# Kernel optimization log

Hardware: AMD Instinct MI355X
Metric: run time of the kernel (lower is better)

The kernel has to match this reference:

```python
import jax, jax.numpy as jnp
import numpy as np

N = 100000   # num nodes
E = 1200000  # num edges (avg degree ~12)
D = 64       # emb_dim


def setup_inputs() -> dict:
    key = jax.random.key(0)
    k1, k2, k3, k4, k5, k6 = jax.random.split(key, 6)
    x = jax.random.normal(k1, (N, D), dtype=jnp.float32)
    edge_index = jax.random.randint(k2, (2, E), 0, N, dtype=jnp.int64)
    edge_attr = jax.random.normal(k3, (E, D), dtype=jnp.float32)
    W = jax.random.normal(k4, (D, D), dtype=jnp.float32) * 0.05  # Linear weight
    b = jax.random.normal(k5, (D,), dtype=jnp.float32) * 0.05    # Linear bias
    root_emb = jax.random.normal(k6, (D,), dtype=jnp.float32)
    return {"x": x, "edge_index": edge_index, "edge_attr": edge_attr,
            "W": W, "b": b, "root_emb": root_emb}


def reference(x, edge_index, edge_attr, W, b, root_emb):
    n = x.shape[0]
    x = x @ W.T + b  # Linear(emb_dim, emb_dim)
    row, col = edge_index[0], edge_index[1]
    ones_e = jnp.ones(row.shape[0], dtype=x.dtype)
    # degrees initialized to ones then index_add of ones per edge endpoint
    deg_i = 1.0 + jax.ops.segment_sum(ones_e, row, num_segments=n)
    deg_j = 1.0 + jax.ops.segment_sum(ones_e, col, num_segments=n)
    dinv_i = deg_i ** -0.5
    dinv_j = deg_j ** -0.5
    val = dinv_i[row] * dinv_j[col]  # [E] normalized edge weights
    # spmm(adj_t, x) + message_edge both scatter val-weighted terms to `row`;
    # fuse into a single gather->scale->segment_sum pass (identical math).
    agg = jax.ops.segment_sum(val[:, None] * (x[col] + edge_attr), row,
                              num_segments=n)  # [N, D]
    node_feat = jax.nn.relu(agg) + jax.nn.relu(x + root_emb) * (dinv_i * dinv_j)[:, None]
    return node_feat
```

## Files before the change

### kernel.cpp

```cpp
#include <hip/hip_runtime.h>

#define N_NODES 100000
#define N_EDGES 1200000
#define DIM     64
#define SCAN_B  256
#define NB      ((N_NODES + SCAN_B - 1) / SCAN_B)
#define LIN_ROWS   32
#define LIN_BLOCKS (N_NODES / LIN_ROWS)
#define CNT_BLOCKS ((N_EDGES / 4 + 255) / 256)

typedef unsigned short ushort_t;
typedef float f4 __attribute__((ext_vector_type(4)));

__device__ inline float bf2f(ushort_t u) {
    return __uint_as_float(((unsigned int)u) << 16);
}
__device__ inline ushort_t f2bf(float f) {
    unsigned int x = __float_as_uint(f);
    unsigned int r = x + 0x7fff + ((x >> 16) & 1);
    return (ushort_t)(r >> 16);
}

__global__ __launch_bounds__(256) void prep_kernel(
        const float* __restrict__ x, const float* __restrict__ W,
        const float* __restrict__ b, ushort_t* __restrict__ xwb,
        const int* __restrict__ row, const int* __restrict__ col,
        int* __restrict__ cnt_r, int* __restrict__ cnt_c,
        int* __restrict__ rank) {
    __shared__ float sWt[DIM * (DIM + 1)];
    __shared__ f4    sx4[LIN_ROWS][DIM / 4];

    int t = threadIdx.x;

    if (blockIdx.x >= LIN_BLOCKS) {
        int i = (blockIdx.x - LIN_BLOCKS) * 256 + t;
        if (i * 4 >= N_EDGES) return;
        int4 r4 = ((const int4*)row)[i];
        int4 c4 = ((const int4*)col)[i];
        int4 rk;
        rk.x = atomicAdd(&cnt_r[r4.x], 1);
        rk.y = atomicAdd(&cnt_r[r4.y], 1);
        rk.z = atomicAdd(&cnt_r[r4.z], 1);
        rk.w = atomicAdd(&cnt_r[r4.w], 1);
        ((int4*)rank)[i] = rk;
        atomicAdd(&cnt_c[c4.x], 1);
        atomicAdd(&cnt_c[c4.y], 1);
        atomicAdd(&cnt_c[c4.z], 1);
        atomicAdd(&cnt_c[c4.w], 1);
        return;
    }

    int row0 = blockIdx.x * LIN_ROWS;
    for (int i = t; i < DIM * DIM; i += 256) {
        int d = i >> 6, k = i & 63;
        sWt[k * (DIM + 1) + d] = W[i];
    }
    for (int i = t; i < LIN_ROWS * (DIM / 4); i += 256) {
        int r = i >> 4, kq = i & 15;
        sx4[r][kq] = __builtin_nontemporal_load(
            (const f4*)(x + (size_t)(row0 + r) * DIM + (kq << 2)));
    }
    __syncthreads();

    int d  = t & 63;
    int rg = (t >> 6) * 8;

    float bd = b[d];
    float a[8];
    #pragma unroll
    for (int r = 0; r < 8; r++) a[r] = bd;

    #pragma unroll
    for (int kq = 0; kq < DIM / 4; kq++) {
        float w0 = sWt[(4 * kq + 0) * (DIM + 1) + d];
        float w1 = sWt[(4 * kq + 1) * (DIM + 1) + d];
        float w2 = sWt[(4 * kq + 2) * (DIM + 1) + d];
        float w3 = sWt[(4 * kq + 3) * (DIM + 1) + d];
        #pragma unroll
        for (int r = 0; r < 8; r++) {
            f4 v = sx4[rg + r][kq];
            a[r] = fmaf(v.w, w3, fmaf(v.z, w2, fmaf(v.y, w1, fmaf(v.x, w0, a[r]))));
        }
    }
    #pragma unroll
    for (int r = 0; r < 8; r++)
        xwb[(size_t)(row0 + rg + r) * DIM + d] = f2bf(a[r]);
}

__global__ void scan_a(const int* __restrict__ cnt_r, const int* __restrict__ cnt_c,
                       int* __restrict__ offsets, int* __restrict__ partials,
                       float* __restrict__ dinv_i, float* __restrict__ dinv_j) {
    __shared__ int s[SCAN_B];
    int t = threadIdx.x;
    int i = blockIdx.x * SCAN_B + t;
    int v = (i < N_NODES) ? cnt_r[i] : 0;
    if (i < N_NODES) {
        dinv_i[i] = rsqrtf(1.0f + (float)v);
        dinv_j[i] = rsqrtf(1.0f + (float)cnt_c[i]);
    }
    s[t] = v;
    __syncthreads();
    for (int off = 1; off < SCAN_B; off <<= 1) {
        int add = (t >= off) ? s[t - off] : 0;
        __syncthreads();
        s[t] += add;
        __syncthreads();
    }
    if (i < N_NODES) offsets[i] = s[t] - v;
    if (t == SCAN_B - 1) partials[blockIdx.x] = s[t];
}

__global__ void scan_c(int* __restrict__ offsets, const int* __restrict__ partials) {
    __shared__ int sred[SCAN_B];
    int t = threadIdx.x, bid = blockIdx.x;
    int v = 0;
    for (int j = t; j < NB; j += SCAN_B)
        if (j < bid) v += partials[j];
    sred[t] = v;
    __syncthreads();
    for (int off = SCAN_B / 2; off > 0; off >>= 1) {
        if (t < off) sred[t] += sred[t + off];
        __syncthreads();
    }
    int base = sred[0];
    int i = bid * SCAN_B + t;
    if (i < N_NODES) offsets[i] += base;
}

__global__ void bin_kernel(const int* __restrict__ row, const int* __restrict__ col,
                           const int* __restrict__ rank, const int* __restrict__ offsets,
                           int2* __restrict__ rec) {
    int i = blockIdx.x * blockDim.x + threadIdx.x;
    if (i * 4 >= N_EDGES) return;
    int4 r4 = ((const int4*)row)[i];
    int4 c4 = ((const int4*)col)[i];
    int4 k4 = ((const int4*)rank)[i];
    int e = i * 4;
    rec[offsets[r4.x] + k4.x] = make_int2(e + 0, c4.x);
    rec[offsets[r4.y] + k4.y] = make_int2(e + 1, c4.y);
    rec[offsets[r4.z] + k4.z] = make_int2(e + 2, c4.z);
    rec[offsets[r4.w] + k4.w] = make_int2(e + 3, c4.w);
}

__global__ __launch_bounds__(256) void gather_kernel(
        const int* __restrict__ offsets, const int* __restrict__ cnt_r,
        const int2* __restrict__ rec,
        const float* __restrict__ edge_attr, const ushort_t* __restrict__ xwb,
        const float* __restrict__ dinv_i, const float* __restrict__ dinv_j,
        const float* __restrict__ root, float* __restrict__ out) {
    int lane = threadIdx.x & 63;
    int g    = lane >> 4;
    int q    = (lane & 15) << 2;
    int n    = blockIdx.x * 4 + (threadIdx.x >> 6);

    int   start = offsets[n];
    int   cnt   = cnt_r[n];
    float di    = dinv_i[n];

    const ushort4 xun0 = *(const ushort4*)(xwb + (size_t)n * DIM + q);
    const f4      rt   = *(const f4*)(root + q);
    const float   vj0  = dinv_j[n];

    f4 acc = {0.f, 0.f, 0.f, 0.f};
    int k = g;
    if (k < cnt) {
        int2 rc0 = rec[start + k];
        int2 rc1 = rec[start + k + 4];
        int2 rc2 = rec[start + k + 8];
        f4 ea0 = __builtin_nontemporal_load(
            (const f4*)(edge_attr + (size_t)rc0.x * DIM + q));
        ushort4 xu0 = *(const ushort4*)(xwb + (size_t)rc0.y * DIM + q);
        float   vjA = dinv_j[rc0.y];
        bool m1 = (k + 4) < cnt;
        f4 ea1; ushort4 xu1; float vjB;
        if (m1) {
            ea1 = __builtin_nontemporal_load(
                (const f4*)(edge_attr + (size_t)rc1.x * DIM + q));
            xu1 = *(const ushort4*)(xwb + (size_t)rc1.y * DIM + q);
            vjB = dinv_j[rc1.y];
        }
        for (;;) {
            bool m2 = (k + 8) < cnt;
            int2 rc3 = rec[start + k + 12];
            f4 ea2; ushort4 xu2; float vjC;
            if (m2) {
                ea2 = __builtin_nontemporal_load(
                    (const f4*)(edge_attr + (size_t)rc2.x * DIM + q));
                xu2 = *(const ushort4*)(xwb + (size_t)rc2.y * DIM + q);
                vjC = dinv_j[rc2.y];
            }
            float vv = di * vjA;
            acc.x = fmaf(vv, ea0.x + bf2f(xu0.x), acc.x);
            acc.y = fmaf(vv, ea0.y + bf2f(xu0.y), acc.y);
            acc.z = fmaf(vv, ea0.z + bf2f(xu0.z), acc.z);
            acc.w = fmaf(vv, ea0.w + bf2f(xu0.w), acc.w);
            if (!m1) break;
            k += 4;
            ea0 = ea1; xu0 = xu1; vjA = vjB;
            ea1 = ea2; xu1 = xu2; vjB = vjC;
            m1 = m2; rc2 = rc3;
        }
    }

    acc.x += __shfl_xor(acc.x, 16); acc.y += __shfl_xor(acc.y, 16);
    acc.z += __shfl_xor(acc.z, 16); acc.w += __shfl_xor(acc.w, 16);
    acc.x += __shfl_xor(acc.x, 32); acc.y += __shfl_xor(acc.y, 32);
    acc.z += __shfl_xor(acc.z, 32); acc.w += __shfl_xor(acc.w, 32);

    if (g == 0) {
        float s = di * vj0;
        f4 o;
        o.x = fmaxf(acc.x, 0.f) + fmaxf(bf2f(xun0.x) + rt.x, 0.f) * s;
        o.y = fmaxf(acc.y, 0.f) + fmaxf(bf2f(xun0.y) + rt.y, 0.f) * s;
        o.z = fmaxf(acc.z, 0.f) + fmaxf(bf2f(xun0.z) + rt.z, 0.f) * s;
        o.w = fmaxf(acc.w, 0.f) + fmaxf(bf2f(xun0.w) + rt.w, 0.f) * s;
        __builtin_nontemporal_store(o, (f4*)(out + (size_t)n * DIM + q));
    }
}

extern "C" void kernel_launch(void* const* d_in, const int* in_sizes, int n_in,
                              void* d_out, int out_size, void* d_ws, size_t ws_size,
                              hipStream_t stream) {
    const float* x         = (const float*)d_in[0];
    const int*   edge_idx  = (const int*)d_in[1];
    const float* edge_attr = (const float*)d_in[2];
    const float* W         = (const float*)d_in[3];
    const float* b         = (const float*)d_in[4];
    const float* root_emb  = (const float*)d_in[5];
    float*       out       = (float*)d_out;

    const int* row = edge_idx;
    const int* col = edge_idx + N_EDGES;

    char* ws = (char*)d_ws;
    ushort_t* xwb      = (ushort_t*)ws;   ws += (size_t)N_NODES * DIM * 2;
    int*      cnt_r    = (int*)ws;        ws += (size_t)N_NODES * 4;
    int*      cnt_c    = (int*)ws;        ws += (size_t)N_NODES * 4;
    float*    dinv_i   = (float*)ws;      ws += (size_t)N_NODES * 4;
    float*    dinv_j   = (float*)ws;      ws += (size_t)N_NODES * 4;
    int*      offsets  = (int*)ws;        ws += (size_t)N_NODES * 4;
    int*      partials = (int*)ws;        ws += 1024 * 4;
    int*      rank     = (int*)ws;        ws += (size_t)N_EDGES * 4;
    int2*     rec      = (int2*)ws;       ws += (size_t)N_EDGES * 8;

    hipMemsetAsync(cnt_r, 0, (size_t)N_NODES * 2 * sizeof(int), stream);

    prep_kernel<<<LIN_BLOCKS + CNT_BLOCKS, 256, 0, stream>>>(
        x, W, b, xwb, row, col, cnt_r, cnt_c, rank);

    scan_a<<<NB, SCAN_B, 0, stream>>>(cnt_r, cnt_c, offsets, partials, dinv_i, dinv_j);
    scan_c<<<NB, SCAN_B, 0, stream>>>(offsets, partials);

    bin_kernel<<<CNT_BLOCKS, 256, 0, stream>>>(row, col, rank, offsets, rec);

    gather_kernel<<<N_NODES / 4, 256, 0, stream>>>(
        offsets, cnt_r, rec, edge_attr, xwb, dinv_i, dinv_j, root_emb, out);
}
```

Measured before the change: 601.1 us.

## Precompute per-edge weights in binning pass and co-schedule linear with binning

Moves the linear-projection blocks out of the counting kernel and fuses them with the binning kernel, so counting runs alone and the GEMM overlaps with the scatter. The binning pass now also writes a CSR-ordered per-edge weight array (dinv_i[row]*dinv_j[col]), so the gather loop reads a sequential value instead of doing a random dinv_j lookup per edge. This adds an extra E-sized float array to write and read, and adds random dinv reads during binning.

```diff
diff --git a/kernel.cpp b/kernel.cpp
--- a/kernel.cpp
+++ b/kernel.cpp
@@ -21,36 +21,101 @@
     return (ushort_t)(r >> 16);
 }
 
-__global__ __launch_bounds__(256) void prep_kernel(
-        const float* __restrict__ x, const float* __restrict__ W,
-        const float* __restrict__ b, ushort_t* __restrict__ xwb,
+__global__ __launch_bounds__(256) void count_kernel(
         const int* __restrict__ row, const int* __restrict__ col,
         int* __restrict__ cnt_r, int* __restrict__ cnt_c,
         int* __restrict__ rank) {
+    int i = blockIdx.x * 256 + threadIdx.x;
+    if (i * 4 >= N_EDGES) return;
+    int4 r4 = ((const int4*)row)[i];
+    int4 c4 = ((const int4*)col)[i];
+    int4 rk;
+    rk.x = atomicAdd(&cnt_r[r4.x], 1);
+    rk.y = atomicAdd(&cnt_r[r4.y], 1);
+    rk.z = atomicAdd(&cnt_r[r4.z], 1);
+    rk.w = atomicAdd(&cnt_r[r4.w], 1);
+    ((int4*)rank)[i] = rk;
+    atomicAdd(&cnt_c[c4.x], 1);
+    atomicAdd(&cnt_c[c4.y], 1);
+    atomicAdd(&cnt_c[c4.z], 1);
+    atomicAdd(&cnt_c[c4.w], 1);
+}
+
+__global__ void scan_a(const int* __restrict__ cnt_r, const int* __restrict__ cnt_c,
+                       int* __restrict__ offsets, int* __restrict__ partials,
+                       float* __restrict__ dinv_i, float* __restrict__ dinv_j) {
+    __shared__ int s[SCAN_B];
+    int t = threadIdx.x;
+    int i = blockIdx.x * SCAN_B + t;
+    int v = (i < N_NODES) ? cnt_r[i] : 0;
+    if (i < N_NODES) {
+        dinv_i[i] = rsqrtf(1.0f + (float)v);
+        dinv_j[i] = rsqrtf(1.0f + (float)cnt_c[i]);
+    }
+    s[t] = v;
+    __syncthreads();
+    for (int off = 1; off < SCAN_B; off <<= 1) {
+        int add = (t >= off) ? s[t - off] : 0;
+        __syncthreads();
+        s[t] += add;
+        __syncthreads();
+    }
+    if (i < N_NODES) offsets[i] = s[t] - v;
+    if (t == SCAN_B - 1) partials[blockIdx.x] = s[t];
+}
+
+__global__ void scan_c(int* __restrict__ offsets, const int* __restrict__ partials) {
+    __shared__ int sred[SCAN_B];
+    int t = threadIdx.x, bid = blockIdx.x;
+    int v = 0;
+    for (int j = t; j < NB; j += SCAN_B)
+        if (j < bid) v += partials[j];
+    sred[t] = v;
+    __syncthreads();
+    for (int off = SCAN_B / 2; off > 0; off >>= 1) {
+        if (t < off) sred[t] += sred[t + off];
+        __syncthreads();
+    }
+    int base = sred[0];
+    int i = bid * SCAN_B + t;
+    if (i < N_NODES) offsets[i] += base;
+}
+
+__global__ __launch_bounds__(256) void binlin_kernel(
+        const int* __restrict__ row, const int* __restrict__ col,
+        const int* __restrict__ rank, const int* __restrict__ offsets,
+        const float* __restrict__ dinv_i, const float* __restrict__ dinv_j,
+        int2* __restrict__ rec, float* __restrict__ val,
+        const float* __restrict__ x, const float* __restrict__ W,
+        const float* __restrict__ b, ushort_t* __restrict__ xwb) {
     __shared__ float sWt[DIM * (DIM + 1)];
     __shared__ f4    sx4[LIN_ROWS][DIM / 4];
 
     int t = threadIdx.x;
 
-    if (blockIdx.x >= LIN_BLOCKS) {
-        int i = (blockIdx.x - LIN_BLOCKS) * 256 + t;
+    if (blockIdx.x < CNT_BLOCKS) {
+        int i = blockIdx.x * 256 + t;
         if (i * 4 >= N_EDGES) return;
         int4 r4 = ((const int4*)row)[i];
         int4 c4 = ((const int4*)col)[i];
-        int4 rk;
-        rk.x = atomicAdd(&cnt_r[r4.x], 1);
-        rk.y = atomicAdd(&cnt_r[r4.y], 1);
-        rk.z = atomicAdd(&cnt_r[r4.z], 1);
-        rk.w = atomicAdd(&cnt_r[r4.w], 1);
-        ((int4*)rank)[i] = rk;
-        atomicAdd(&cnt_c[c4.x], 1);
-        atomicAdd(&cnt_c[c4.y], 1);
-        atomicAdd(&cnt_c[c4.z], 1);
-        atomicAdd(&cnt_c[c4.w], 1);
+        int4 k4 = ((const int4*)rank)[i];
+        int e = i * 4;
+        int p0 = offsets[r4.x] + k4.x;
+        int p1 = offsets[r4.y] + k4.y;
+        int p2 = offsets[r4.z] + k4.z;
+        int p3 = offsets[r4.w] + k4.w;
+        rec[p0] = make_int2(e + 0, c4.x);
+        rec[p1] = make_int2(e + 1, c4.y);
+        rec[p2] = make_int2(e + 2, c4.z);
+        rec[p3] = make_int2(e + 3, c4.w);
+        val[p0] = dinv_i[r4.x] * dinv_j[c4.x];
+        val[p1] = dinv_i[r4.y] * dinv_j[c4.y];
+        val[p2] = dinv_i[r4.z] * dinv_j[c4.z];
+        val[p3] = dinv_i[r4.w] * dinv_j[c4.w];
         return;
     }
 
-    int row0 = blockIdx.x * LIN_ROWS;
+    int row0 = (blockIdx.x - CNT_BLOCKS) * LIN_ROWS;
     for (int i = t; i < DIM * DIM; i += 256) {
         int d = i >> 6, k = i & 63;
         sWt[k * (DIM + 1) + d] = W[i];
@@ -87,64 +152,9 @@
         xwb[(size_t)(row0 + rg + r) * DIM + d] = f2bf(a[r]);
 }
 
-__global__ void scan_a(const int* __restrict__ cnt_r, const int* __restrict__ cnt_c,
-                       int* __restrict__ offsets, int* __restrict__ partials,
-                       float* __restrict__ dinv_i, float* __restrict__ dinv_j) {
-    __shared__ int s[SCAN_B];
-    int t = threadIdx.x;
-    int i = blockIdx.x * SCAN_B + t;
-    int v = (i < N_NODES) ? cnt_r[i] : 0;
-    if (i < N_NODES) {
-        dinv_i[i] = rsqrtf(1.0f + (float)v);
-        dinv_j[i] = rsqrtf(1.0f + (float)cnt_c[i]);
-    }
-    s[t] = v;
-    __syncthreads();
-    for (int off = 1; off < SCAN_B; off <<= 1) {
-        int add = (t >= off) ? s[t - off] : 0;
-        __syncthreads();
-        s[t] += add;
-        __syncthreads();
-    }
-    if (i < N_NODES) offsets[i] = s[t] - v;
-    if (t == SCAN_B - 1) partials[blockIdx.x] = s[t];
-}
-
-__global__ void scan_c(int* __restrict__ offsets, const int* __restrict__ partials) {
-    __shared__ int sred[SCAN_B];
-    int t = threadIdx.x, bid = blockIdx.x;
-    int v = 0;
-    for (int j = t; j < NB; j += SCAN_B)
-        if (j < bid) v += partials[j];
-    sred[t] = v;
-    __syncthreads();
-    for (int off = SCAN_B / 2; off > 0; off >>= 1) {
-        if (t < off) sred[t] += sred[t + off];
-        __syncthreads();
-    }
-    int base = sred[0];
-    int i = bid * SCAN_B + t;
-    if (i < N_NODES) offsets[i] += base;
-}
-
-__global__ void bin_kernel(const int* __restrict__ row, const int* __restrict__ col,
-                           const int* __restrict__ rank, const int* __restrict__ offsets,
-                           int2* __restrict__ rec) {
-    int i = blockIdx.x * blockDim.x + threadIdx.x;
-    if (i * 4 >= N_EDGES) return;
-    int4 r4 = ((const int4*)row)[i];
-    int4 c4 = ((const int4*)col)[i];
-    int4 k4 = ((const int4*)rank)[i];
-    int e = i * 4;
-    rec[offsets[r4.x] + k4.x] = make_int2(e + 0, c4.x);
-    rec[offsets[r4.y] + k4.y] = make_int2(e + 1, c4.y);
-    rec[offsets[r4.z] + k4.z] = make_int2(e + 2, c4.z);
-    rec[offsets[r4.w] + k4.w] = make_int2(e + 3, c4.w);
-}
-
 __global__ __launch_bounds__(256) void gather_kernel(
         const int* __restrict__ offsets, const int* __restrict__ cnt_r,
-        const int2* __restrict__ rec,
+        const int2* __restrict__ rec, const float* __restrict__ val,
         const float* __restrict__ edge_attr, const ushort_t* __restrict__ xwb,
         const float* __restrict__ dinv_i, const float* __restrict__ dinv_j,
         const float* __restrict__ root, float* __restrict__ out) {
@@ -164,40 +174,40 @@
     f4 acc = {0.f, 0.f, 0.f, 0.f};
     int k = g;
     if (k < cnt) {
-        int2 rc0 = rec[start + k];
-        int2 rc1 = rec[start + k + 4];
-        int2 rc2 = rec[start + k + 8];
+        int2  rc0 = rec[start + k];
+        float v0  = val[start + k];
+        int2  rc1 = rec[start + k + 4];
+        float v1  = val[start + k + 4];
+        int2  rc2 = rec[start + k + 8];
+        float v2  = val[start + k + 8];
         f4 ea0 = __builtin_nontemporal_load(
             (const f4*)(edge_attr + (size_t)rc0.x * DIM + q));
         ushort4 xu0 = *(const ushort4*)(xwb + (size_t)rc0.y * DIM + q);
-        float   vjA = dinv_j[rc0.y];
         bool m1 = (k + 4) < cnt;
-        f4 ea1; ushort4 xu1; float vjB;
+        f4 ea1; ushort4 xu1;
         if (m1) {
             ea1 = __builtin_nontemporal_load(
                 (const f4*)(edge_attr + (size_t)rc1.x * DIM + q));
             xu1 = *(const ushort4*)(xwb + (size_t)rc1.y * DIM + q);
-            vjB = dinv_j[rc1.y];
         }
         for (;;) {
-            bool m2 = (k + 8) < cnt;
-            int2 rc3 = rec[start + k + 12];
-            f4 ea2; ushort4 xu2; float vjC;
+            bool  m2  = (k + 8) < cnt;
+            int2  rc3 = rec[start + k + 12];
+            float v3  = val[start + k + 12];
+            f4 ea2; ushort4 xu2;
             if (m2) {
                 ea2 = __builtin_nontemporal_load(
                     (const f4*)(edge_attr + (size_t)rc2.x * DIM + q));
                 xu2 = *(const ushort4*)(xwb + (size_t)rc2.y * DIM + q);
-                vjC = dinv_j[rc2.y];
             }
-            float vv = di * vjA;
-            acc.x = fmaf(vv, ea0.x + bf2f(xu0.x), acc.x);
-            acc.y = fmaf(vv, ea0.y + bf2f(xu0.y), acc.y);
-            acc.z = fmaf(vv, ea0.z + bf2f(xu0.z), acc.z);
-            acc.w = fmaf(vv, ea0.w + bf2f(xu0.w), acc.w);
+            acc.x = fmaf(v0, ea0.x + bf2f(xu0.x), acc.x);
+            acc.y = fmaf(v0, ea0.y + bf2f(xu0.y), acc.y);
+            acc.z = fmaf(v0, ea0.z + bf2f(xu0.z), acc.z);
+            acc.w = fmaf(v0, ea0.w + bf2f(xu0.w), acc.w);
             if (!m1) break;
             k += 4;
-            ea0 = ea1; xu0 = xu1; vjA = vjB;
-            ea1 = ea2; xu1 = xu2; vjB = vjC;
+            ea0 = ea1; xu0 = xu1; v0 = v1;
+            ea1 = ea2; xu1 = xu2; v1 = v2; v2 = v3;
             m1 = m2; rc2 = rc3;
         }
     }
@@ -241,18 +251,19 @@
     int*      offsets  = (int*)ws;        ws += (size_t)N_NODES * 4;
     int*      partials = (int*)ws;        ws += 1024 * 4;
     int*      rank     = (int*)ws;        ws += (size_t)N_EDGES * 4;
+    float*    val      = (float*)ws;      ws += (size_t)N_EDGES * 4;
     int2*     rec      = (int2*)ws;       ws += (size_t)N_EDGES * 8;
 
     hipMemsetAsync(cnt_r, 0, (size_t)N_NODES * 2 * sizeof(int), stream);
 
-    prep_kernel<<<LIN_BLOCKS + CNT_BLOCKS, 256, 0, stream>>>(
-        x, W, b, xwb, row, col, cnt_r, cnt_c, rank);
+    count_kernel<<<CNT_BLOCKS, 256, 0, stream>>>(row, col, cnt_r, cnt_c, rank);
 
     scan_a<<<NB, SCAN_B, 0, stream>>>(cnt_r, cnt_c, offsets, partials, dinv_i, dinv_j);
     scan_c<<<NB, SCAN_B, 0, stream>>>(offsets, partials);
 
-    bin_kernel<<<CNT_BLOCKS, 256, 0, stream>>>(row, col, rank, offsets, rec);
+    binlin_kernel<<<CNT_BLOCKS + LIN_BLOCKS, 256, 0, stream>>>(
+        row, col, rank, offsets, dinv_i, dinv_j, rec, val, x, W, b, xwb);
 
     gather_kernel<<<N_NODES / 4, 256, 0, stream>>>(
-        offsets, cnt_r, rec, edge_attr, xwb, dinv_i, dinv_j, root_emb, out);
-}
+        offsets, cnt_r, rec, val, edge_attr, xwb, dinv_i, dinv_j, root_emb, out);
+}
```

After: 612.1 us. No clear change (+1.8%).
